# Kernel optimization log

Hardware: AMD Instinct MI355X
Metric: run time of the kernel (lower is better)

The kernel has to match this reference:

```python
import jax, jax.numpy as jnp
import numpy as np

N_HEAD = 8
LN_EPS = 1e-6


def setup_inputs() -> dict:
    key = jax.random.key(0)
    ks = jax.random.split(key, 6)
    B, S, D = 4, 2048, 256  # D = hidden_size*2 = input_dim
    sc = 1.0 / np.sqrt(D)
    return {
        "inputs": jax.random.normal(ks[0], (B, S, D), jnp.float32),
        "Wq": jax.random.normal(ks[1], (D, D), jnp.float32) * sc,
        "Wk": jax.random.normal(ks[2], (D, D), jnp.float32) * sc,
        "Wv": jax.random.normal(ks[3], (D, D), jnp.float32) * sc,
        "Wf": jax.random.normal(ks[4], (D, D), jnp.float32) * sc,
        "bf": jnp.zeros((D,), jnp.float32),
        "gamma": jnp.ones((D,), jnp.float32),
        "beta": jnp.zeros((D,), jnp.float32),
    }


def reference(inputs, Wq, Wk, Wv, Wf, bf, gamma, beta):
    B, S, D = inputs.shape
    H = N_HEAD
    dh = D // H
    # Projections (torch Linear: x @ W.T), no bias for Q/K/V
    Q = (inputs @ Wq.T).reshape(B, S, H, dh)
    K = (inputs @ Wk.T).reshape(B, S, H, dh)
    V = (inputs @ Wv.T).reshape(B, S, H, dh)
    # NOTE: original scales by sqrt(K.shape[1]) == sqrt(seq_len), not sqrt(dh)
    scale = 1.0 / jnp.sqrt(jnp.float32(S)).astype(inputs.dtype)
    scores = jnp.einsum("bqhd,bkhd->bhqk", Q, K) * scale  # [B,H,S,S]
    attn = jax.nn.softmax(scores, axis=-1)
    out = jnp.einsum("bhqk,bkhd->bqhd", attn, V).reshape(B, S, D)
    out = out @ Wf.T + bf
    # residual + LayerNorm(eps=1e-6)
    x = inputs + out
    mu = jnp.mean(x, axis=-1, keepdims=True)
    var = jnp.mean(jnp.square(x - mu), axis=-1, keepdims=True)
    return (x - mu) * jax.lax.rsqrt(var + LN_EPS) * gamma + beta
```

## Files before the change

### kernel.cpp

```cpp
#include <hip/hip_runtime.h>
#include <hip/hip_bf16.h>

typedef __attribute__((ext_vector_type(8))) short short8;
typedef __attribute__((ext_vector_type(4))) float f32x4;
typedef __attribute__((ext_vector_type(16))) float f32x16;

#define DEVI __device__ __forceinline__

DEVI unsigned short f2bf(float f) {
  union { float f; unsigned int u; } v; v.f = f;
  unsigned int r = v.u + 0x7fffu + ((v.u >> 16) & 1u);
  return (unsigned short)(r >> 16);
}

#define GLDS16(gp, lp)                                                         \
  __builtin_amdgcn_global_load_lds(                                            \
      (const __attribute__((address_space(1))) unsigned int*)(uintptr_t)(gp),  \
      (__attribute__((address_space(3))) unsigned int*)(uintptr_t)(lp), 16, 0, 0)

#define SB 4
#define SS 2048
#define SD 256
#define SH 8
#define SDH 32
#define SM 8192

#define QSCALE 0.0318793654f

#define XBF_OFF 0
#define W_OFF   (SM * SD)
#define Q_OFF   (W_OFF + 4 * SD * SD)
#define K_OFF   (Q_OFF + SM * SD)
#define VT_OFF  (K_OFF + SM * SD)
#define AO_OFF  (VT_OFF + SM * SD)

__global__ __launch_bounds__(256) void convert_k(
    const float* __restrict__ X, const float* __restrict__ Wq,
    const float* __restrict__ Wk, const float* __restrict__ Wv,
    const float* __restrict__ Wf, unsigned short* __restrict__ ws) {
  const int XN = SM * SD;
  const int WN = SD * SD;
  int i4 = (blockIdx.x * 256 + threadIdx.x) * 4;
  const float* src; unsigned short* dst; int idx;
  if (i4 < XN)             { src = X;  dst = ws + XBF_OFF;      idx = i4; }
  else if (i4 < XN + WN)   { src = Wq; dst = ws + W_OFF;        idx = i4 - XN; }
  else if (i4 < XN + 2*WN) { src = Wk; dst = ws + W_OFF + WN;   idx = i4 - XN - WN; }
  else if (i4 < XN + 3*WN) { src = Wv; dst = ws + W_OFF + 2*WN; idx = i4 - XN - 2*WN; }
  else if (i4 < XN + 4*WN) { src = Wf; dst = ws + W_OFF + 3*WN; idx = i4 - XN - 3*WN; }
  else return;
  float4 v = *reinterpret_cast<const float4*>(src + idx);
  unsigned short o[4] = { f2bf(v.x), f2bf(v.y), f2bf(v.z), f2bf(v.w) };
  *reinterpret_cast<uint2*>(dst + idx) = *reinterpret_cast<const uint2*>(o);
}

__global__ __launch_bounds__(256) void qkv_k(const unsigned short* __restrict__ ws_c,
                                             unsigned short* __restrict__ ws) {
  __shared__ __align__(16) unsigned short Atile[128][72];
  __shared__ __align__(16) unsigned short Btile[128][72];
  const unsigned short* Xb = ws_c + XBF_OFF;
  const unsigned short* Wall = ws_c + W_OFF;
  int tid = threadIdx.x, w = tid >> 6, lane = tid & 63, g = lane >> 4, r = lane & 15;
  int m0 = blockIdx.x * 128, n0 = blockIdx.y * 128;
  int wr = (w >> 1) * 64, wc = (w & 1) * 64;
  f32x4 acc[4][4] = {};
  int srow = tid >> 3, scol = (tid & 7) * 8;
  short8 a[4], b[4];
#pragma unroll
  for (int p = 0; p < 4; ++p) {
    a[p] = *reinterpret_cast<const short8*>(Xb + (m0 + srow + p * 32) * SD + scol);
    b[p] = *reinterpret_cast<const short8*>(Wall + (n0 + srow + p * 32) * SD + scol);
  }
  for (int k0 = 0; k0 < SD; k0 += 64) {
    __syncthreads();
#pragma unroll
    for (int p = 0; p < 4; ++p) {
      *reinterpret_cast<short8*>(&Atile[srow + p * 32][scol]) = a[p];
      *reinterpret_cast<short8*>(&Btile[srow + p * 32][scol]) = b[p];
    }
    __syncthreads();
    if (k0 + 64 < SD) {
#pragma unroll
      for (int p = 0; p < 4; ++p) {
        a[p] = *reinterpret_cast<const short8*>(Xb + (m0 + srow + p * 32) * SD + k0 + 64 + scol);
        b[p] = *reinterpret_cast<const short8*>(Wall + (n0 + srow + p * 32) * SD + k0 + 64 + scol);
      }
    }
#pragma unroll
    for (int ks = 0; ks < 2; ++ks) {
      short8 af[4], bf[4];
#pragma unroll
      for (int i = 0; i < 4; ++i)
        af[i] = *reinterpret_cast<const short8*>(&Atile[wr + i * 16 + r][ks * 32 + g * 8]);
#pragma unroll
      for (int j = 0; j < 4; ++j)
        bf[j] = *reinterpret_cast<const short8*>(&Btile[wc + j * 16 + r][ks * 32 + g * 8]);
#pragma unroll
      for (int i = 0; i < 4; ++i)
#pragma unroll
        for (int j = 0; j < 4; ++j)
          acc[i][j] = __builtin_amdgcn_mfma_f32_16x16x32_bf16(af[i], bf[j], acc[i][j], 0, 0, 0);
    }
  }
  int z = n0 >> 8;
  int nbase = n0 & 255;
  int b_ = m0 >> 11, sbase = m0 & 2047;
  float qs = (z == 0) ? QSCALE : 1.0f;
  unsigned short* Vt = &Btile[0][0];
#pragma unroll
  for (int p = 0; p < 2; ++p) {
    __syncthreads();
    if ((w & 1) == p) {
      if (z < 2) {
#pragma unroll
        for (int i = 0; i < 4; ++i)
#pragma unroll
          for (int j = 0; j < 4; ++j)
#pragma unroll
            for (int jj = 0; jj < 4; ++jj)
              Atile[wr + i * 16 + g * 4 + jj][j * 16 + r] = f2bf(acc[i][j][jj] * qs);
      } else {
#pragma unroll
        for (int i = 0; i < 4; ++i)
#pragma unroll
          for (int j = 0; j < 4; ++j) {
            unsigned short o4[4];
#pragma unroll
            for (int jj = 0; jj < 4; ++jj) o4[jj] = f2bf(acc[i][j][jj]);
            *reinterpret_cast<uint2*>(&Vt[(j * 16 + r) * 136 + wr + i * 16 + g * 4]) =
                *reinterpret_cast<const uint2*>(o4);
          }
      }
    }
    __syncthreads();
    if (z < 2) {
      unsigned short* out = ws + (z == 0 ? Q_OFF : K_OFF);
      int h0 = (nbase + p * 64) >> 5;
#pragma unroll
      for (int it = 0; it < 4; ++it) {
        int c = it * 256 + tid;
        int m = c >> 3, cr = c & 7, hl = cr >> 2, ch = cr & 3;
        short8 val = *reinterpret_cast<const short8*>(&Atile[m][hl * 32 + ch * 8]);
        int h = h0 + hl;
        *reinterpret_cast<short8*>(
            out + (((b_ << 3) + h) * SS + sbase + m) * SDH + ch * 8) = val;
      }
    } else {
      unsigned short* out = ws + VT_OFF;
      int nb = nbase + p * 64;
#pragma unroll
      for (int it = 0; it < 4; ++it) {
        int c = it * 256 + tid;
        int nl = c >> 4, ch = c & 15;
        short8 val = *reinterpret_cast<const short8*>(&Vt[nl * 136 + ch * 8]);
        int col = nb + nl, h = col >> 5, d = col & 31;
        *reinterpret_cast<short8*>(
            out + ((((b_ << 3) + h) << 5) + d) * SS + sbase + ch * 8) = val;
      }
    }
  }
}

__global__ __launch_bounds__(512, 4) void attn_k(const unsigned short* __restrict__ ws_c,
                                                 unsigned short* __restrict__ ws) {
  __shared__ __align__(16) unsigned short Kb[2][2][64 * 32];
  __shared__ __align__(16) unsigned short Vb[2][2][32 * 64];
  int tid = threadIdx.x, w = tid >> 6, lane = tid & 63;
  int wg = w >> 2, wl = w & 3, gtid = tid & 255;
  int n32 = lane & 31, hi = lane >> 5;
  int wgid = ((blockIdx.x & 7) << 6) + (blockIdx.x >> 3);
  int bh = wgid >> 4, qb = wgid & 15;
  int q0 = qb * 128 + wl * 32;
  const unsigned short* Qh = ws_c + Q_OFF + bh * (SS * SDH);
  const unsigned short* Kg = ws_c + K_OFF + (bh * SS + wg * 1024) * SDH;
  const unsigned short* Vg = ws_c + VT_OFF + bh * (SDH * SS) + wg * 1024;
  short8 qB0 = *reinterpret_cast<const short8*>(Qh + (q0 + n32) * SDH + 8 * hi);
  short8 qB1 = *reinterpret_cast<const short8*>(Qh + (q0 + n32) * SDH + 16 + 8 * hi);
  int krow = gtid >> 2, kch = (gtid & 3) ^ (krow & 3);
  const unsigned short* gK = Kg + krow * SDH + kch * 8;
  int vrow = gtid >> 3, vch = (gtid & 7) ^ (vrow & 7);
  const unsigned short* gV = Vg + vrow * SS + vch * 8;
  int wv = gtid >> 6;
  unsigned short* lK[2] = { &Kb[wg][0][wv * 512], &Kb[wg][1][wv * 512] };
  unsigned short* lV[2] = { &Vb[wg][0][wv * 512], &Vb[wg][1][wv * 512] };
  GLDS16(gK, lK[0]);
  GLDS16(gV, lV[0]);
  f32x16 O = {};
  float Lacc = 0.f;
  for (int t = 0; t < 16; ++t) {
    const unsigned short* Kbase = &Kb[wg][t & 1][0];
    const unsigned short* Vbase = &Vb[wg][t & 1][0];
    if (t < 15) {
      GLDS16(gK + (t + 1) * 64 * SDH, lK[(t + 1) & 1]);
      GLDS16(gV + (t + 1) * 64, lV[(t + 1) & 1]);
      asm volatile("s_waitcnt vmcnt(2)" ::: "memory");
    } else {
      asm volatile("s_waitcnt vmcnt(0)" ::: "memory");
    }
    __builtin_amdgcn_s_barrier();
    short8 kA00 = *reinterpret_cast<const short8*>(Kbase + n32 * 32 + ((hi ^ (n32 & 3)) * 8));
    short8 kA01 = *reinterpret_cast<const short8*>(Kbase + n32 * 32 + (((2 + hi) ^ (n32 & 3)) * 8));
    short8 kA10 = *reinterpret_cast<const short8*>(Kbase + (32 + n32) * 32 + ((hi ^ (n32 & 3)) * 8));
    short8 kA11 = *reinterpret_cast<const short8*>(Kbase + (32 + n32) * 32 + (((2 + hi) ^ (n32 & 3)) * 8));
    f32x16 a0 = {}, a1 = {};
    __builtin_amdgcn_s_setprio(1);
    a0 = __builtin_amdgcn_mfma_f32_32x32x16_bf16(kA00, qB0, a0, 0, 0, 0);
    a1 = __builtin_amdgcn_mfma_f32_32x32x16_bf16(kA10, qB0, a1, 0, 0, 0);
    a0 = __builtin_amdgcn_mfma_f32_32x32x16_bf16(kA01, qB1, a0, 0, 0, 0);
    a1 = __builtin_amdgcn_mfma_f32_32x32x16_bf16(kA11, qB1, a1, 0, 0, 0);
    __builtin_amdgcn_s_setprio(0);
#pragma unroll
    for (int i = 0; i < 16; ++i) a0[i] = __builtin_amdgcn_exp2f(a0[i]);
#pragma unroll
    for (int i = 0; i < 16; ++i) a1[i] = __builtin_amdgcn_exp2f(a1[i]);
    float s0 = 0.f, s1 = 0.f;
#pragma unroll
    for (int i = 0; i < 8; ++i) { s0 += a0[2 * i] + a1[2 * i]; s1 += a0[2 * i + 1] + a1[2 * i + 1]; }
    Lacc += s0 + s1;
    unsigned int pk0[8], pk1[8];
#pragma unroll
    for (int i = 0; i < 8; ++i) {
      unsigned int r0, r1;
      asm("v_cvt_pk_bf16_f32 %0, %1, %2" : "=v"(r0) : "v"(a0[2 * i]), "v"(a0[2 * i + 1]));
      asm("v_cvt_pk_bf16_f32 %0, %1, %2" : "=v"(r1) : "v"(a1[2 * i]), "v"(a1[2 * i + 1]));
      pk0[i] = r0; pk1[i] = r1;
    }
    asm("v_permlane32_swap_b32 %0, %1" : "+v"(pk0[0]), "+v"(pk0[2]));
    asm("v_permlane32_swap_b32 %0, %1" : "+v"(pk0[1]), "+v"(pk0[3]));
    asm("v_permlane32_swap_b32 %0, %1" : "+v"(pk0[4]), "+v"(pk0[6]));
    asm("v_permlane32_swap_b32 %0, %1" : "+v"(pk0[5]), "+v"(pk0[7]));
    asm("v_permlane32_swap_b32 %0, %1" : "+v"(pk1[0]), "+v"(pk1[2]));
    asm("v_permlane32_swap_b32 %0, %1" : "+v"(pk1[1]), "+v"(pk1[3]));
    asm("v_permlane32_swap_b32 %0, %1" : "+v"(pk1[4]), "+v"(pk1[6]));
    asm("v_permlane32_swap_b32 %0, %1" : "+v"(pk1[5]), "+v"(pk1[7]));
    union { unsigned int u[4]; short8 sv; } A10, A20, A11, A21;
    A10.u[0] = pk0[0]; A10.u[1] = pk0[1]; A10.u[2] = pk0[2]; A10.u[3] = pk0[3];
    A20.u[0] = pk0[4]; A20.u[1] = pk0[5]; A20.u[2] = pk0[6]; A20.u[3] = pk0[7];
    A11.u[0] = pk1[0]; A11.u[1] = pk1[1]; A11.u[2] = pk1[2]; A11.u[3] = pk1[3];
    A21.u[0] = pk1[4]; A21.u[1] = pk1[5]; A21.u[2] = pk1[6]; A21.u[3] = pk1[7];
    short8 vB00 = *reinterpret_cast<const short8*>(Vbase + n32 * 64 + ((hi ^ (n32 & 7)) * 8));
    short8 vB01 = *reinterpret_cast<const short8*>(Vbase + n32 * 64 + (((2 + hi) ^ (n32 & 7)) * 8));
    short8 vB10 = *reinterpret_cast<const short8*>(Vbase + n32 * 64 + (((4 + hi) ^ (n32 & 7)) * 8));
    short8 vB11 = *reinterpret_cast<const short8*>(Vbase + n32 * 64 + (((6 + hi) ^ (n32 & 7)) * 8));
    __builtin_amdgcn_s_setprio(1);
    O = __builtin_amdgcn_mfma_f32_32x32x16_bf16(A10.sv, vB00, O, 0, 0, 0);
    O = __builtin_amdgcn_mfma_f32_32x32x16_bf16(A20.sv, vB01, O, 0, 0, 0);
    O = __builtin_amdgcn_mfma_f32_32x32x16_bf16(A11.sv, vB10, O, 0, 0, 0);
    O = __builtin_amdgcn_mfma_f32_32x32x16_bf16(A21.sv, vB11, O, 0, 0, 0);
    __builtin_amdgcn_s_setprio(0);
    __builtin_amdgcn_s_barrier();
  }
  __syncthreads();
  float* OCp = reinterpret_cast<float*>(&Kb[0][0][0]);
  float* LCp = reinterpret_cast<float*>(&Vb[0][0][0]);
  if (wg == 1) {
#pragma unroll
    for (int i = 0; i < 16; ++i) OCp[(wl * 64 + lane) * 16 + i] = O[i];
    LCp[wl * 64 + lane] = Lacc;
  }
  __syncthreads();
  if (wg == 0) {
#pragma unroll
    for (int i = 0; i < 16; ++i) O[i] += OCp[(wl * 64 + lane) * 16 + i];
    Lacc += LCp[wl * 64 + lane];
    float Lt = Lacc + __shfl_xor(Lacc, 32);
    float* Linv = LCp + 256 + wl * 32;
    if (lane < 32) Linv[n32] = 1.0f / Lt;
    int b = bh >> 3, h = bh & 7;
    unsigned short* AO = ws + AO_OFF;
#pragma unroll
    for (int rr = 0; rr < 16; ++rr) {
      int q = (rr & 3) + 8 * (rr >> 2) + 4 * hi;
      AO[(b * SS + q0 + q) * SD + h * SDH + n32] = f2bf(O[rr] * Linv[q]);
    }
  }
}

__global__ __launch_bounds__(256) void final_k(
    const unsigned short* __restrict__ ws_c, const float* __restrict__ X,
    const float* __restrict__ bfv, const float* __restrict__ gamma,
    const float* __restrict__ beta, float* __restrict__ out) {
  __shared__ __align__(16) unsigned short Al[32][72];
  __shared__ __align__(16) unsigned short Bl[256][72];
  __shared__ float Cl[32][257];
  const unsigned short* AO = ws_c + AO_OFF;
  const unsigned short* Wf = ws_c + W_OFF + 3 * (SD * SD);
  int tid = threadIdx.x, w = tid >> 6, lane = tid & 63, g = lane >> 4, r = lane & 15;
  int m0 = blockIdx.x * 32;
  f32x4 acc[2][4] = {};
  int arow = tid >> 3, acol = (tid & 7) * 8;
  for (int k0 = 0; k0 < SD; k0 += 64) {
    short8 av = *reinterpret_cast<const short8*>(AO + (m0 + arow) * SD + k0 + acol);
    short8 bv[8];
#pragma unroll
    for (int i = 0; i < 8; i++)
      bv[i] = *reinterpret_cast<const short8*>(Wf + (i * 32 + arow) * SD + k0 + acol);
    __syncthreads();
    *reinterpret_cast<short8*>(&Al[arow][acol]) = av;
#pragma unroll
    for (int i = 0; i < 8; i++)
      *reinterpret_cast<short8*>(&Bl[i * 32 + arow][acol]) = bv[i];
    __syncthreads();
#pragma unroll
    for (int ks = 0; ks < 2; ks++) {
      short8 af0 = *reinterpret_cast<const short8*>(&Al[r][ks * 32 + g * 8]);
      short8 af1 = *reinterpret_cast<const short8*>(&Al[16 + r][ks * 32 + g * 8]);
#pragma unroll
      for (int nt = 0; nt < 4; nt++) {
        short8 bb = *reinterpret_cast<const short8*>(&Bl[w * 64 + nt * 16 + r][ks * 32 + g * 8]);
        acc[0][nt] = __builtin_amdgcn_mfma_f32_16x16x32_bf16(af0, bb, acc[0][nt], 0, 0, 0);
        acc[1][nt] = __builtin_amdgcn_mfma_f32_16x16x32_bf16(af1, bb, acc[1][nt], 0, 0, 0);
      }
    }
  }
#pragma unroll
  for (int rt = 0; rt < 2; rt++)
#pragma unroll
    for (int nt = 0; nt < 4; nt++)
#pragma unroll
      for (int j = 0; j < 4; j++)
        Cl[rt * 16 + g * 4 + j][w * 64 + nt * 16 + r] = acc[rt][nt][j];
  __syncthreads();
  int row = tid >> 3, sub = tid & 7;
  int m = m0 + row;
  float x[32];
  float sum = 0.f, sumsq = 0.f;
#pragma unroll
  for (int i = 0; i < 8; i++) {
    int col = sub * 32 + i * 4;
    float4 xv = *reinterpret_cast<const float4*>(X + m * SD + col);
    float4 bb = *reinterpret_cast<const float4*>(bfv + col);
    x[i * 4 + 0] = Cl[row][col + 0] + xv.x + bb.x;
    x[i * 4 + 1] = Cl[row][col + 1] + xv.y + bb.y;
    x[i * 4 + 2] = Cl[row][col + 2] + xv.z + bb.z;
    x[i * 4 + 3] = Cl[row][col + 3] + xv.w + bb.w;
  }
#pragma unroll
  for (int c = 0; c < 32; c++) { sum += x[c]; sumsq += x[c] * x[c]; }
  sum += __shfl_xor(sum, 1);  sumsq += __shfl_xor(sumsq, 1);
  sum += __shfl_xor(sum, 2);  sumsq += __shfl_xor(sumsq, 2);
  sum += __shfl_xor(sum, 4);  sumsq += __shfl_xor(sumsq, 4);
  float mean = sum * (1.0f / 256.0f);
  float var = sumsq * (1.0f / 256.0f) - mean * mean;
  float rstd = rsqrtf(var + 1e-6f);
#pragma unroll
  for (int i = 0; i < 8; i++) {
    int col = sub * 32 + i * 4;
    float4 gv = *reinterpret_cast<const float4*>(gamma + col);
    float4 bv2 = *reinterpret_cast<const float4*>(beta + col);
    float4 ov;
    ov.x = (x[i * 4 + 0] - mean) * rstd * gv.x + bv2.x;
    ov.y = (x[i * 4 + 1] - mean) * rstd * gv.y + bv2.y;
    ov.z = (x[i * 4 + 2] - mean) * rstd * gv.z + bv2.z;
    ov.w = (x[i * 4 + 3] - mean) * rstd * gv.w + bv2.w;
    *reinterpret_cast<float4*>(out + m * SD + col) = ov;
  }
}

extern "C" void kernel_launch(void* const* d_in, const int* in_sizes, int n_in,
                              void* d_out, int out_size, void* d_ws, size_t ws_size,
                              hipStream_t stream) {
  const float* X  = (const float*)d_in[0];
  const float* Wq = (const float*)d_in[1];
  const float* Wk = (const float*)d_in[2];
  const float* Wv = (const float*)d_in[3];
  const float* Wf = (const float*)d_in[4];
  const float* bf = (const float*)d_in[5];
  const float* gm = (const float*)d_in[6];
  const float* bt = (const float*)d_in[7];
  float* out = (float*)d_out;
  unsigned short* ws = (unsigned short*)d_ws;

  convert_k<<<2304, 256, 0, stream>>>(X, Wq, Wk, Wv, Wf, ws);
  qkv_k<<<dim3(64, 6), 256, 0, stream>>>(ws, ws);
  attn_k<<<dim3(512), 512, 0, stream>>>(ws, ws);
  final_k<<<256, 256, 0, stream>>>(ws, X, bf, gm, bt, out);
}
```

Before: 59.09 us.

## Fuse fp32-to-bf16 conversion into GEMMs and enlarge attention KV tiles

Removes the separate conversion kernel: the QKV projection and the final projection now load fp32 inputs and weights directly and pack them to bf16 with v_cvt_pk_bf16_f32 before writing to LDS. This saves one launch and a full write/read round trip of the bf16 copy of the input. The attention kernel now stages 128-key tiles (8 iterations instead of 16) with a new swizzle and four async loads per stage. The softmax row sum is computed by MFMA against a ones vector instead of VALU adds and a shuffle. Risks include more fp32 global traffic per GEMM tile, extra MFMA work for the row sum, and higher LDS use.

```diff
diff --git a/kernel.cpp b/kernel.cpp
--- a/kernel.cpp
+++ b/kernel.cpp
@@ -11,6 +11,12 @@
   union { float f; unsigned int u; } v; v.f = f;
   unsigned int r = v.u + 0x7fffu + ((v.u >> 16) & 1u);
   return (unsigned short)(r >> 16);
+}
+
+DEVI unsigned int cvt2(float lo, float hi) {
+  unsigned int r;
+  asm("v_cvt_pk_bf16_f32 %0, %1, %2" : "=v"(r) : "v"(lo), "v"(hi));
+  return r;
 }
 
 #define GLDS16(gp, lp)                                                         \
@@ -27,62 +33,55 @@
 
 #define QSCALE 0.0318793654f
 
-#define XBF_OFF 0
-#define W_OFF   (SM * SD)
-#define Q_OFF   (W_OFF + 4 * SD * SD)
-#define K_OFF   (Q_OFF + SM * SD)
-#define VT_OFF  (K_OFF + SM * SD)
-#define AO_OFF  (VT_OFF + SM * SD)
-
-__global__ __launch_bounds__(256) void convert_k(
+#define Q_OFF   0
+#define K_OFF   (SM * SD)
+#define VT_OFF  (2 * SM * SD)
+#define AO_OFF  (3 * SM * SD)
+
+__global__ __launch_bounds__(256) void qkv_k(
     const float* __restrict__ X, const float* __restrict__ Wq,
     const float* __restrict__ Wk, const float* __restrict__ Wv,
-    const float* __restrict__ Wf, unsigned short* __restrict__ ws) {
-  const int XN = SM * SD;
-  const int WN = SD * SD;
-  int i4 = (blockIdx.x * 256 + threadIdx.x) * 4;
-  const float* src; unsigned short* dst; int idx;
-  if (i4 < XN)             { src = X;  dst = ws + XBF_OFF;      idx = i4; }
-  else if (i4 < XN + WN)   { src = Wq; dst = ws + W_OFF;        idx = i4 - XN; }
-  else if (i4 < XN + 2*WN) { src = Wk; dst = ws + W_OFF + WN;   idx = i4 - XN - WN; }
-  else if (i4 < XN + 3*WN) { src = Wv; dst = ws + W_OFF + 2*WN; idx = i4 - XN - 2*WN; }
-  else if (i4 < XN + 4*WN) { src = Wf; dst = ws + W_OFF + 3*WN; idx = i4 - XN - 3*WN; }
-  else return;
-  float4 v = *reinterpret_cast<const float4*>(src + idx);
-  unsigned short o[4] = { f2bf(v.x), f2bf(v.y), f2bf(v.z), f2bf(v.w) };
-  *reinterpret_cast<uint2*>(dst + idx) = *reinterpret_cast<const uint2*>(o);
-}
-
-__global__ __launch_bounds__(256) void qkv_k(const unsigned short* __restrict__ ws_c,
-                                             unsigned short* __restrict__ ws) {
+    unsigned short* __restrict__ ws) {
   __shared__ __align__(16) unsigned short Atile[128][72];
   __shared__ __align__(16) unsigned short Btile[128][72];
-  const unsigned short* Xb = ws_c + XBF_OFF;
-  const unsigned short* Wall = ws_c + W_OFF;
   int tid = threadIdx.x, w = tid >> 6, lane = tid & 63, g = lane >> 4, r = lane & 15;
   int m0 = blockIdx.x * 128, n0 = blockIdx.y * 128;
+  int z = n0 >> 8, nbase = n0 & 255;
+  const float* Wz = (z == 0) ? Wq : (z == 1) ? Wk : Wv;
   int wr = (w >> 1) * 64, wc = (w & 1) * 64;
   f32x4 acc[4][4] = {};
   int srow = tid >> 3, scol = (tid & 7) * 8;
-  short8 a[4], b[4];
+  float4 a0[4], a1[4], b0[4], b1[4];
 #pragma unroll
   for (int p = 0; p < 4; ++p) {
-    a[p] = *reinterpret_cast<const short8*>(Xb + (m0 + srow + p * 32) * SD + scol);
-    b[p] = *reinterpret_cast<const short8*>(Wall + (n0 + srow + p * 32) * SD + scol);
+    const float* xa = X + (m0 + srow + p * 32) * SD + scol;
+    const float* xb = Wz + (nbase + srow + p * 32) * SD + scol;
+    a0[p] = *reinterpret_cast<const float4*>(xa);
+    a1[p] = *reinterpret_cast<const float4*>(xa + 4);
+    b0[p] = *reinterpret_cast<const float4*>(xb);
+    b1[p] = *reinterpret_cast<const float4*>(xb + 4);
   }
   for (int k0 = 0; k0 < SD; k0 += 64) {
     __syncthreads();
 #pragma unroll
     for (int p = 0; p < 4; ++p) {
-      *reinterpret_cast<short8*>(&Atile[srow + p * 32][scol]) = a[p];
-      *reinterpret_cast<short8*>(&Btile[srow + p * 32][scol]) = b[p];
+      uint4 ua = { cvt2(a0[p].x, a0[p].y), cvt2(a0[p].z, a0[p].w),
+                   cvt2(a1[p].x, a1[p].y), cvt2(a1[p].z, a1[p].w) };
+      uint4 ub = { cvt2(b0[p].x, b0[p].y), cvt2(b0[p].z, b0[p].w),
+                   cvt2(b1[p].x, b1[p].y), cvt2(b1[p].z, b1[p].w) };
+      *reinterpret_cast<uint4*>(&Atile[srow + p * 32][scol]) = ua;
+      *reinterpret_cast<uint4*>(&Btile[srow + p * 32][scol]) = ub;
     }
     __syncthreads();
     if (k0 + 64 < SD) {
 #pragma unroll
       for (int p = 0; p < 4; ++p) {
-        a[p] = *reinterpret_cast<const short8*>(Xb + (m0 + srow + p * 32) * SD + k0 + 64 + scol);
-        b[p] = *reinterpret_cast<const short8*>(Wall + (n0 + srow + p * 32) * SD + k0 + 64 + scol);
+        const float* xa = X + (m0 + srow + p * 32) * SD + k0 + 64 + scol;
+        const float* xb = Wz + (nbase + srow + p * 32) * SD + k0 + 64 + scol;
+        a0[p] = *reinterpret_cast<const float4*>(xa);
+        a1[p] = *reinterpret_cast<const float4*>(xa + 4);
+        b0[p] = *reinterpret_cast<const float4*>(xb);
+        b1[p] = *reinterpret_cast<const float4*>(xb + 4);
       }
     }
 #pragma unroll
@@ -101,8 +100,6 @@
           acc[i][j] = __builtin_amdgcn_mfma_f32_16x16x32_bf16(af[i], bf[j], acc[i][j], 0, 0, 0);
     }
   }
-  int z = n0 >> 8;
-  int nbase = n0 & 255;
   int b_ = m0 >> 11, sbase = m0 & 2047;
   float qs = (z == 0) ? QSCALE : 1.0f;
   unsigned short* Vt = &Btile[0][0];
@@ -162,8 +159,7 @@
 
 __global__ __launch_bounds__(512, 4) void attn_k(const unsigned short* __restrict__ ws_c,
                                                  unsigned short* __restrict__ ws) {
-  __shared__ __align__(16) unsigned short Kb[2][2][64 * 32];
-  __shared__ __align__(16) unsigned short Vb[2][2][32 * 64];
+  __shared__ __align__(16) unsigned char smem[65536];
   int tid = threadIdx.x, w = tid >> 6, lane = tid & 63;
   int wg = w >> 2, wl = w & 3, gtid = tid & 255;
   int n32 = lane & 31, hi = lane >> 5;
@@ -175,130 +171,155 @@
   const unsigned short* Vg = ws_c + VT_OFF + bh * (SDH * SS) + wg * 1024;
   short8 qB0 = *reinterpret_cast<const short8*>(Qh + (q0 + n32) * SDH + 8 * hi);
   short8 qB1 = *reinterpret_cast<const short8*>(Qh + (q0 + n32) * SDH + 16 + 8 * hi);
-  int krow = gtid >> 2, kch = (gtid & 3) ^ (krow & 3);
-  const unsigned short* gK = Kg + krow * SDH + kch * 8;
-  int vrow = gtid >> 3, vch = (gtid & 7) ^ (vrow & 7);
-  const unsigned short* gV = Vg + vrow * SS + vch * 8;
+  unsigned short* Kbuf0 = (unsigned short*)(smem + wg * 16384);
+  unsigned short* Kbuf1 = (unsigned short*)(smem + wg * 16384 + 8192);
+  unsigned short* Vbuf0 = (unsigned short*)(smem + 32768 + wg * 16384);
+  unsigned short* Vbuf1 = (unsigned short*)(smem + 32768 + wg * 16384 + 8192);
   int wv = gtid >> 6;
-  unsigned short* lK[2] = { &Kb[wg][0][wv * 512], &Kb[wg][1][wv * 512] };
-  unsigned short* lV[2] = { &Vb[wg][0][wv * 512], &Vb[wg][1][wv * 512] };
-  GLDS16(gK, lK[0]);
-  GLDS16(gV, lV[0]);
-  f32x16 O = {};
-  float Lacc = 0.f;
-  for (int t = 0; t < 16; ++t) {
-    const unsigned short* Kbase = &Kb[wg][t & 1][0];
-    const unsigned short* Vbase = &Vb[wg][t & 1][0];
-    if (t < 15) {
-      GLDS16(gK + (t + 1) * 64 * SDH, lK[(t + 1) & 1]);
-      GLDS16(gV + (t + 1) * 64, lV[(t + 1) & 1]);
-      asm volatile("s_waitcnt vmcnt(2)" ::: "memory");
+  int kr = gtid >> 2;
+  int kcg = (gtid & 3) ^ ((kr >> 1) & 3);
+  const unsigned short* gK0 = Kg + kr * SDH + kcg * 8;
+  const unsigned short* gK1 = gK0 + 64 * SDH;
+  int vr = gtid >> 4;
+  int vcg = (gtid & 15) ^ (vr & 7);
+  const unsigned short* gV0 = Vg + vr * SS + vcg * 8;
+  const unsigned short* gV1 = gV0 + 16 * SS;
+  auto issue = [&](int buf, int tt) {
+    char* kd = (char*)(buf ? Kbuf1 : Kbuf0) + wv * 1024;
+    char* vd = (char*)(buf ? Vbuf1 : Vbuf0) + wv * 1024;
+    GLDS16(gK0 + tt * 4096, kd);
+    GLDS16(gK1 + tt * 4096, kd + 4096);
+    GLDS16(gV0 + tt * 128, vd);
+    GLDS16(gV1 + tt * 128, vd + 4096);
+  };
+  issue(0, 0);
+  f32x16 O = {}, Lf = {};
+  union { unsigned int u[4]; short8 sv; } ONES;
+  ONES.u[0] = 0x3F803F80u; ONES.u[1] = 0x3F803F80u;
+  ONES.u[2] = 0x3F803F80u; ONES.u[3] = 0x3F803F80u;
+  int rb = (n32 >> 1) & 3;
+  int koff0 = (hi ^ rb) * 8;
+  int koff1 = ((2 + hi) ^ rb) * 8;
+  int vb7 = n32 & 7;
+  for (int t = 0; t < 8; ++t) {
+    const unsigned short* Kt = (t & 1) ? Kbuf1 : Kbuf0;
+    const unsigned short* Vt = (t & 1) ? Vbuf1 : Vbuf0;
+    if (t < 7) {
+      issue((t + 1) & 1, t + 1);
+      asm volatile("s_waitcnt vmcnt(4)" ::: "memory");
     } else {
       asm volatile("s_waitcnt vmcnt(0)" ::: "memory");
     }
     __builtin_amdgcn_s_barrier();
-    short8 kA00 = *reinterpret_cast<const short8*>(Kbase + n32 * 32 + ((hi ^ (n32 & 3)) * 8));
-    short8 kA01 = *reinterpret_cast<const short8*>(Kbase + n32 * 32 + (((2 + hi) ^ (n32 & 3)) * 8));
-    short8 kA10 = *reinterpret_cast<const short8*>(Kbase + (32 + n32) * 32 + ((hi ^ (n32 & 3)) * 8));
-    short8 kA11 = *reinterpret_cast<const short8*>(Kbase + (32 + n32) * 32 + (((2 + hi) ^ (n32 & 3)) * 8));
-    f32x16 a0 = {}, a1 = {};
-    __builtin_amdgcn_s_setprio(1);
-    a0 = __builtin_amdgcn_mfma_f32_32x32x16_bf16(kA00, qB0, a0, 0, 0, 0);
-    a1 = __builtin_amdgcn_mfma_f32_32x32x16_bf16(kA10, qB0, a1, 0, 0, 0);
-    a0 = __builtin_amdgcn_mfma_f32_32x32x16_bf16(kA01, qB1, a0, 0, 0, 0);
-    a1 = __builtin_amdgcn_mfma_f32_32x32x16_bf16(kA11, qB1, a1, 0, 0, 0);
-    __builtin_amdgcn_s_setprio(0);
-#pragma unroll
-    for (int i = 0; i < 16; ++i) a0[i] = __builtin_amdgcn_exp2f(a0[i]);
-#pragma unroll
-    for (int i = 0; i < 16; ++i) a1[i] = __builtin_amdgcn_exp2f(a1[i]);
-    float s0 = 0.f, s1 = 0.f;
-#pragma unroll
-    for (int i = 0; i < 8; ++i) { s0 += a0[2 * i] + a1[2 * i]; s1 += a0[2 * i + 1] + a1[2 * i + 1]; }
-    Lacc += s0 + s1;
-    unsigned int pk0[8], pk1[8];
-#pragma unroll
-    for (int i = 0; i < 8; ++i) {
-      unsigned int r0, r1;
-      asm("v_cvt_pk_bf16_f32 %0, %1, %2" : "=v"(r0) : "v"(a0[2 * i]), "v"(a0[2 * i + 1]));
-      asm("v_cvt_pk_bf16_f32 %0, %1, %2" : "=v"(r1) : "v"(a1[2 * i]), "v"(a1[2 * i + 1]));
-      pk0[i] = r0; pk1[i] = r1;
-    }
-    asm("v_permlane32_swap_b32 %0, %1" : "+v"(pk0[0]), "+v"(pk0[2]));
-    asm("v_permlane32_swap_b32 %0, %1" : "+v"(pk0[1]), "+v"(pk0[3]));
-    asm("v_permlane32_swap_b32 %0, %1" : "+v"(pk0[4]), "+v"(pk0[6]));
-    asm("v_permlane32_swap_b32 %0, %1" : "+v"(pk0[5]), "+v"(pk0[7]));
-    asm("v_permlane32_swap_b32 %0, %1" : "+v"(pk1[0]), "+v"(pk1[2]));
-    asm("v_permlane32_swap_b32 %0, %1" : "+v"(pk1[1]), "+v"(pk1[3]));
-    asm("v_permlane32_swap_b32 %0, %1" : "+v"(pk1[4]), "+v"(pk1[6]));
-    asm("v_permlane32_swap_b32 %0, %1" : "+v"(pk1[5]), "+v"(pk1[7]));
-    union { unsigned int u[4]; short8 sv; } A10, A20, A11, A21;
-    A10.u[0] = pk0[0]; A10.u[1] = pk0[1]; A10.u[2] = pk0[2]; A10.u[3] = pk0[3];
-    A20.u[0] = pk0[4]; A20.u[1] = pk0[5]; A20.u[2] = pk0[6]; A20.u[3] = pk0[7];
-    A11.u[0] = pk1[0]; A11.u[1] = pk1[1]; A11.u[2] = pk1[2]; A11.u[3] = pk1[3];
-    A21.u[0] = pk1[4]; A21.u[1] = pk1[5]; A21.u[2] = pk1[6]; A21.u[3] = pk1[7];
-    short8 vB00 = *reinterpret_cast<const short8*>(Vbase + n32 * 64 + ((hi ^ (n32 & 7)) * 8));
-    short8 vB01 = *reinterpret_cast<const short8*>(Vbase + n32 * 64 + (((2 + hi) ^ (n32 & 7)) * 8));
-    short8 vB10 = *reinterpret_cast<const short8*>(Vbase + n32 * 64 + (((4 + hi) ^ (n32 & 7)) * 8));
-    short8 vB11 = *reinterpret_cast<const short8*>(Vbase + n32 * 64 + (((6 + hi) ^ (n32 & 7)) * 8));
-    __builtin_amdgcn_s_setprio(1);
-    O = __builtin_amdgcn_mfma_f32_32x32x16_bf16(A10.sv, vB00, O, 0, 0, 0);
-    O = __builtin_amdgcn_mfma_f32_32x32x16_bf16(A20.sv, vB01, O, 0, 0, 0);
-    O = __builtin_amdgcn_mfma_f32_32x32x16_bf16(A11.sv, vB10, O, 0, 0, 0);
-    O = __builtin_amdgcn_mfma_f32_32x32x16_bf16(A21.sv, vB11, O, 0, 0, 0);
-    __builtin_amdgcn_s_setprio(0);
+#pragma unroll
+    for (int batch = 0; batch < 2; ++batch) {
+      int sub0 = batch * 2, sub1 = batch * 2 + 1;
+      const unsigned short* kr0 = Kt + (sub0 * 32 + n32) * 32;
+      const unsigned short* kr1 = Kt + (sub1 * 32 + n32) * 32;
+      short8 kA00 = *reinterpret_cast<const short8*>(kr0 + koff0);
+      short8 kA01 = *reinterpret_cast<const short8*>(kr0 + koff1);
+      short8 kA10 = *reinterpret_cast<const short8*>(kr1 + koff0);
+      short8 kA11 = *reinterpret_cast<const short8*>(kr1 + koff1);
+      f32x16 a0 = {}, a1 = {};
+      __builtin_amdgcn_s_setprio(1);
+      a0 = __builtin_amdgcn_mfma_f32_32x32x16_bf16(kA00, qB0, a0, 0, 0, 0);
+      a1 = __builtin_amdgcn_mfma_f32_32x32x16_bf16(kA10, qB0, a1, 0, 0, 0);
+      a0 = __builtin_amdgcn_mfma_f32_32x32x16_bf16(kA01, qB1, a0, 0, 0, 0);
+      a1 = __builtin_amdgcn_mfma_f32_32x32x16_bf16(kA11, qB1, a1, 0, 0, 0);
+      __builtin_amdgcn_s_setprio(0);
+#pragma unroll
+      for (int i = 0; i < 16; ++i) a0[i] = __builtin_amdgcn_exp2f(a0[i]);
+#pragma unroll
+      for (int i = 0; i < 16; ++i) a1[i] = __builtin_amdgcn_exp2f(a1[i]);
+      unsigned int pk0[8], pk1[8];
+#pragma unroll
+      for (int i = 0; i < 8; ++i) {
+        pk0[i] = cvt2(a0[2 * i], a0[2 * i + 1]);
+        pk1[i] = cvt2(a1[2 * i], a1[2 * i + 1]);
+      }
+      asm("v_permlane32_swap_b32 %0, %1" : "+v"(pk0[0]), "+v"(pk0[2]));
+      asm("v_permlane32_swap_b32 %0, %1" : "+v"(pk0[1]), "+v"(pk0[3]));
+      asm("v_permlane32_swap_b32 %0, %1" : "+v"(pk0[4]), "+v"(pk0[6]));
+      asm("v_permlane32_swap_b32 %0, %1" : "+v"(pk0[5]), "+v"(pk0[7]));
+      asm("v_permlane32_swap_b32 %0, %1" : "+v"(pk1[0]), "+v"(pk1[2]));
+      asm("v_permlane32_swap_b32 %0, %1" : "+v"(pk1[1]), "+v"(pk1[3]));
+      asm("v_permlane32_swap_b32 %0, %1" : "+v"(pk1[4]), "+v"(pk1[6]));
+      asm("v_permlane32_swap_b32 %0, %1" : "+v"(pk1[5]), "+v"(pk1[7]));
+      union { unsigned int u[4]; short8 sv; } A10, A20, A11, A21;
+      A10.u[0] = pk0[0]; A10.u[1] = pk0[1]; A10.u[2] = pk0[2]; A10.u[3] = pk0[3];
+      A20.u[0] = pk0[4]; A20.u[1] = pk0[5]; A20.u[2] = pk0[6]; A20.u[3] = pk0[7];
+      A11.u[0] = pk1[0]; A11.u[1] = pk1[1]; A11.u[2] = pk1[2]; A11.u[3] = pk1[3];
+      A21.u[0] = pk1[4]; A21.u[1] = pk1[5]; A21.u[2] = pk1[6]; A21.u[3] = pk1[7];
+      const unsigned short* vrow = Vt + n32 * 128;
+      short8 vB00 = *reinterpret_cast<const short8*>(vrow + ((sub0 * 4 + hi) ^ vb7) * 8);
+      short8 vB01 = *reinterpret_cast<const short8*>(vrow + ((sub0 * 4 + 2 + hi) ^ vb7) * 8);
+      short8 vB10 = *reinterpret_cast<const short8*>(vrow + ((sub1 * 4 + hi) ^ vb7) * 8);
+      short8 vB11 = *reinterpret_cast<const short8*>(vrow + ((sub1 * 4 + 2 + hi) ^ vb7) * 8);
+      __builtin_amdgcn_s_setprio(1);
+      O = __builtin_amdgcn_mfma_f32_32x32x16_bf16(A10.sv, vB00, O, 0, 0, 0);
+      O = __builtin_amdgcn_mfma_f32_32x32x16_bf16(A20.sv, vB01, O, 0, 0, 0);
+      O = __builtin_amdgcn_mfma_f32_32x32x16_bf16(A11.sv, vB10, O, 0, 0, 0);
+      O = __builtin_amdgcn_mfma_f32_32x32x16_bf16(A21.sv, vB11, O, 0, 0, 0);
+      Lf = __builtin_amdgcn_mfma_f32_32x32x16_bf16(A10.sv, ONES.sv, Lf, 0, 0, 0);
+      Lf = __builtin_amdgcn_mfma_f32_32x32x16_bf16(A20.sv, ONES.sv, Lf, 0, 0, 0);
+      Lf = __builtin_amdgcn_mfma_f32_32x32x16_bf16(A11.sv, ONES.sv, Lf, 0, 0, 0);
+      Lf = __builtin_amdgcn_mfma_f32_32x32x16_bf16(A21.sv, ONES.sv, Lf, 0, 0, 0);
+      __builtin_amdgcn_s_setprio(0);
+    }
     __builtin_amdgcn_s_barrier();
   }
   __syncthreads();
-  float* OCp = reinterpret_cast<float*>(&Kb[0][0][0]);
-  float* LCp = reinterpret_cast<float*>(&Vb[0][0][0]);
+  float* OCf = reinterpret_cast<float*>(smem);
+  float* LCf = OCf + 16 * 257;
+  int p = wl * 64 + lane;
   if (wg == 1) {
 #pragma unroll
-    for (int i = 0; i < 16; ++i) OCp[(wl * 64 + lane) * 16 + i] = O[i];
-    LCp[wl * 64 + lane] = Lacc;
+    for (int i = 0; i < 16; ++i) { OCf[i * 257 + p] = O[i]; LCf[i * 257 + p] = Lf[i]; }
   }
   __syncthreads();
   if (wg == 0) {
-#pragma unroll
-    for (int i = 0; i < 16; ++i) O[i] += OCp[(wl * 64 + lane) * 16 + i];
-    Lacc += LCp[wl * 64 + lane];
-    float Lt = Lacc + __shfl_xor(Lacc, 32);
-    float* Linv = LCp + 256 + wl * 32;
-    if (lane < 32) Linv[n32] = 1.0f / Lt;
     int b = bh >> 3, h = bh & 7;
     unsigned short* AO = ws + AO_OFF;
 #pragma unroll
     for (int rr = 0; rr < 16; ++rr) {
+      float Ot = O[rr] + OCf[rr * 257 + p];
+      float Lt = Lf[rr] + LCf[rr * 257 + p];
       int q = (rr & 3) + 8 * (rr >> 2) + 4 * hi;
-      AO[(b * SS + q0 + q) * SD + h * SDH + n32] = f2bf(O[rr] * Linv[q]);
+      AO[(b * SS + q0 + q) * SD + h * SDH + n32] = f2bf(Ot / Lt);
     }
   }
 }
 
 __global__ __launch_bounds__(256) void final_k(
     const unsigned short* __restrict__ ws_c, const float* __restrict__ X,
-    const float* __restrict__ bfv, const float* __restrict__ gamma,
-    const float* __restrict__ beta, float* __restrict__ out) {
+    const float* __restrict__ Wf, const float* __restrict__ bfv,
+    const float* __restrict__ gamma, const float* __restrict__ beta,
+    float* __restrict__ out) {
   __shared__ __align__(16) unsigned short Al[32][72];
   __shared__ __align__(16) unsigned short Bl[256][72];
   __shared__ float Cl[32][257];
   const unsigned short* AO = ws_c + AO_OFF;
-  const unsigned short* Wf = ws_c + W_OFF + 3 * (SD * SD);
   int tid = threadIdx.x, w = tid >> 6, lane = tid & 63, g = lane >> 4, r = lane & 15;
   int m0 = blockIdx.x * 32;
   f32x4 acc[2][4] = {};
   int arow = tid >> 3, acol = (tid & 7) * 8;
   for (int k0 = 0; k0 < SD; k0 += 64) {
     short8 av = *reinterpret_cast<const short8*>(AO + (m0 + arow) * SD + k0 + acol);
-    short8 bv[8];
-#pragma unroll
-    for (int i = 0; i < 8; i++)
-      bv[i] = *reinterpret_cast<const short8*>(Wf + (i * 32 + arow) * SD + k0 + acol);
+    float4 w0[8], w1[8];
+#pragma unroll
+    for (int i = 0; i < 8; i++) {
+      const float* wp = Wf + (i * 32 + arow) * SD + k0 + acol;
+      w0[i] = *reinterpret_cast<const float4*>(wp);
+      w1[i] = *reinterpret_cast<const float4*>(wp + 4);
+    }
     __syncthreads();
     *reinterpret_cast<short8*>(&Al[arow][acol]) = av;
 #pragma unroll
-    for (int i = 0; i < 8; i++)
-      *reinterpret_cast<short8*>(&Bl[i * 32 + arow][acol]) = bv[i];
+    for (int i = 0; i < 8; i++) {
+      uint4 ub = { cvt2(w0[i].x, w0[i].y), cvt2(w0[i].z, w0[i].w),
+                   cvt2(w1[i].x, w1[i].y), cvt2(w1[i].z, w1[i].w) };
+      *reinterpret_cast<uint4*>(&Bl[i * 32 + arow][acol]) = ub;
+    }
     __syncthreads();
 #pragma unroll
     for (int ks = 0; ks < 2; ks++) {
@@ -370,8 +391,7 @@
   float* out = (float*)d_out;
   unsigned short* ws = (unsigned short*)d_ws;
 
-  convert_k<<<2304, 256, 0, stream>>>(X, Wq, Wk, Wv, Wf, ws);
-  qkv_k<<<dim3(64, 6), 256, 0, stream>>>(ws, ws);
+  qkv_k<<<dim3(64, 6), 256, 0, stream>>>(X, Wq, Wk, Wv, ws);
   attn_k<<<dim3(512), 512, 0, stream>>>(ws, ws);
-  final_k<<<256, 256, 0, stream>>>(ws, X, bf, gm, bt, out);
-}
+  final_k<<<256, 256, 0, stream>>>(ws, X, Wf, bf, gm, bt, out);
+}
```

Result: no change. 58.80 us (-0.5%).
